# Kernel optimization log

Hardware: AMD Instinct MI355X
Metric: run time of the kernel (lower is better)

Reference implementation:

```python
import jax, jax.numpy as jnp
import numpy as np

DET_SIZE = 5120
DET_THRESHOLD = 0.5
NMS_THRESHOLD = 0.4
STRIDES = (8, 16, 32)
NUM_ANCHORS = 2
TOP_K = 2048  # fixed pre-NMS candidate count (jit-friendly stand-in for torch.where filtering)


def _anchor_centers(stride):
    n = DET_SIZE // stride
    g = jnp.arange(n, dtype=jnp.float32) * stride
    X, Y = jnp.meshgrid(g, g, indexing='xy')       # matches torch.meshgrid(..., indexing='xy')
    c = jnp.stack([X, Y], axis=-1).reshape(-1, 2)  # (n*n, 2), x fastest
    return jnp.repeat(c, NUM_ANCHORS, axis=0)      # stack([c]*2, dim=1).reshape(-1,2) == interleaved repeat


def _pairwise_iou(b):
    # b: (K,4) xyxy
    area = jnp.clip(b[:, 2] - b[:, 0], 0.0) * jnp.clip(b[:, 3] - b[:, 1], 0.0)
    lt = jnp.maximum(b[:, None, :2], b[None, :, :2])
    rb = jnp.minimum(b[:, None, 2:], b[None, :, 2:])
    wh = jnp.clip(rb - lt, 0.0)
    inter = wh[..., 0] * wh[..., 1]
    return inter / (area[:, None] + area[None, :] - inter + 1e-9)


def _forward(scores8, bbox8, lms8, scores16, bbox16, lms16, scores32, bbox32, lms32, det_scale):
    confs, boxes, lmss = [], [], []
    per_stride = [(scores8, bbox8, lms8), (scores16, bbox16, lms16), (scores32, bbox32, lms32)]
    for (conf, bbox, lms), stride in zip(per_stride, STRIDES):
        c = _anchor_centers(stride)                 # (N,2)
        b = bbox * stride                            # distance-style offsets scaled by stride
        l = lms * stride
        box = jnp.concatenate([c - b[:, :2], c + b[:, 2:4]], axis=-1) / det_scale  # (N,4) xyxy
        pts = (c[:, None, :] + l.reshape(-1, 5, 2)) / det_scale                    # (N,5,2)
        confs.append(conf.reshape(-1)); boxes.append(box); lmss.append(pts)
    conf = jnp.concatenate(confs)
    box = jnp.concatenate(boxes, axis=0)
    pts = jnp.concatenate(lmss, axis=0)
    # score threshold via masking (fixed shapes); below-threshold entries get conf=-1
    conf_m = jnp.where(conf >= DET_THRESHOLD, conf, -1.0)
    top_conf, top_idx = jax.lax.top_k(conf_m, TOP_K)
    top_box = box[top_idx]          # (K,4)
    top_pts = pts[top_idx]          # (K,5,2)
    valid = top_conf >= DET_THRESHOLD
    iou = _pairwise_iou(top_box)    # (K,K)
    later = jnp.arange(TOP_K)
    def body(i, keep):
        supp = (iou[i] > NMS_THRESHOLD) & (later > i) & keep[i] & valid[i]
        return keep & ~supp
    keep = jax.lax.fori_loop(0, TOP_K, body, valid)  # greedy NMS in descending-score order
    m = keep.astype(top_box.dtype)
    # (K, 15) = [conf | bbox(4) | lms(10)], suppressed/invalid rows zeroed
    return jnp.concatenate([(top_conf * m)[:, None], top_box * m[:, None], top_pts.reshape(TOP_K, 10) * m[:, None]], axis=-1)


def setup_inputs() -> dict:
    key = jax.random.key(0)
    ks = jax.random.split(key, 9)
    inp = {}
    for i, s in enumerate(STRIDES):
        n = DET_SIZE // s
        N = n * n * NUM_ANCHORS
        inp[f'scores{s}'] = jax.random.uniform(ks[3 * i], (N,), dtype=jnp.float32)
        inp[f'bbox{s}'] = jax.random.uniform(ks[3 * i + 1], (N, 4), dtype=jnp.float32) * 8.0
        inp[f'lms{s}'] = jax.random.normal(ks[3 * i + 2], (N, 10), dtype=jnp.float32) * 4.0
    inp['det_scale'] = jnp.array(0.5, dtype=jnp.float32)
    return inp


def reference(scores8, bbox8, lms8, scores16, bbox16, lms16, scores32, bbox32, lms32, det_scale):
    return _forward(scores8, bbox8, lms8, scores16, bbox16, lms16, scores32, bbox32, lms32, det_scale)
```

## Files before the change

### kernel.cpp

```cpp
#include <hip/hip_runtime.h>
#include <stdint.h>
#include <stddef.h>

#pragma clang fp contract(off)

#define N8   819200u
#define N16  204800u
#define N32  51200u
#define NTOT 1075200u
#define TOPK 2048
#define CAND_MAX 8192
#define NBIN 16384u
#define BINSHIFT 9
#define NMS_THR 0.4f
#define DET_THR 0.5f

#define OFF_HIST   0u
#define OFF_META   65536u
#define OFF_CAND   65600u
#define OFF_TIDX   131136u
#define OFF_TCONF  139328u
#define OFF_BOX    147520u
#define OFF_KEEP   180544u
#define OFF_DIAG   180800u
#define OFF_SUPP   188992u

__device__ __forceinline__ float load_conf(unsigned a, const float* __restrict__ s8,
                                           const float* __restrict__ s16,
                                           const float* __restrict__ s32) {
  if (a < N8) return s8[a];
  if (a < N8 + N16) return s16[a - N8];
  return s32[a - (N8 + N16)];
}

__device__ __forceinline__ void decode(unsigned a,
    const float* __restrict__ b8, const float* __restrict__ l8,
    const float* __restrict__ b16, const float* __restrict__ l16,
    const float* __restrict__ b32, const float* __restrict__ l32,
    float& cx, float& cy, float& s, const float*& bb, const float*& lm) {
  if (a < N8) {
    unsigned cell = a >> 1;
    cx = (float)((cell % 640u) * 8u); cy = (float)((cell / 640u) * 8u);
    s = 8.f; bb = b8 + (size_t)a * 4; lm = l8 + (size_t)a * 10;
  } else if (a < N8 + N16) {
    unsigned loc = a - N8; unsigned cell = loc >> 1;
    cx = (float)((cell % 320u) * 16u); cy = (float)((cell / 320u) * 16u);
    s = 16.f; bb = b16 + (size_t)loc * 4; lm = l16 + (size_t)loc * 10;
  } else {
    unsigned loc = a - (N8 + N16); unsigned cell = loc >> 1;
    cx = (float)((cell % 160u) * 32u); cy = (float)((cell / 160u) * 32u);
    s = 32.f; bb = b32 + (size_t)loc * 4; lm = l32 + (size_t)loc * 10;
  }
}

__global__ void k_hist(const float* __restrict__ s8, const float* __restrict__ s16,
                       const float* __restrict__ s32, unsigned* __restrict__ hist) {
  unsigned i = blockIdx.x * blockDim.x + threadIdx.x;
  unsigned st = gridDim.x * blockDim.x;
  for (unsigned a = i; a < NTOT; a += st) {
    float c = load_conf(a, s8, s16, s32);
    if (c >= DET_THR) {
      unsigned v = (__float_as_uint(c) - 0x3F000000u) >> BINSHIFT;
      if (v > NBIN - 1u) v = NBIN - 1u;
      atomicAdd(&hist[v], 1u);
    }
  }
}

__global__ void __launch_bounds__(1024) k_scan(const unsigned* __restrict__ hist,
                                               unsigned* __restrict__ meta) {
  __shared__ unsigned suf[1024];
  int t = threadIdx.x;
  const unsigned* hp = hist + (size_t)t * 16;
  unsigned s = 0;
  for (int b = 0; b < 16; b++) s += hp[b];
  suf[t] = s;
  __syncthreads();
  for (int d = 1; d < 1024; d <<= 1) {
    unsigned v = (t + d < 1024) ? suf[t + d] : 0u;
    __syncthreads();
    suf[t] += v;
    __syncthreads();
  }
  unsigned total = suf[0];
  unsigned mine = suf[t];
  unsigned nxt = (t < 1023) ? suf[t + 1] : 0u;
  if (total < (unsigned)TOPK) {
    if (t == 0) { meta[0] = 0u; meta[2] = total; }
    return;
  }
  if (mine >= (unsigned)TOPK && nxt < (unsigned)TOPK) {
    unsigned run = nxt, cut = (unsigned)t * 16u;
    for (int b = 15; b >= 0; b--) {
      run += hp[b];
      if (run >= (unsigned)TOPK) { cut = (unsigned)t * 16u + (unsigned)b; break; }
    }
    meta[0] = cut; meta[2] = total;
  }
}

__global__ void k_compact(const float* __restrict__ s8, const float* __restrict__ s16,
                          const float* __restrict__ s32, unsigned* __restrict__ meta,
                          unsigned long long* __restrict__ cand) {
  unsigned cut = meta[0];
  unsigned i = blockIdx.x * blockDim.x + threadIdx.x;
  unsigned st = gridDim.x * blockDim.x;
  for (unsigned a = i; a < NTOT; a += st) {
    float c = load_conf(a, s8, s16, s32);
    if (c >= DET_THR) {
      unsigned b = __float_as_uint(c);
      unsigned v = (b - 0x3F000000u) >> BINSHIFT;
      if (v >= cut) {
        unsigned pos = atomicAdd(&meta[3], 1u);
        if (pos < (unsigned)CAND_MAX)
          cand[pos] = ((unsigned long long)b << 32) |
                      (unsigned long long)(0xFFFFFFFFu - a);
      }
    }
  }
}

__global__ void __launch_bounds__(256) k_rank(
    const unsigned long long* __restrict__ cand, const unsigned* __restrict__ meta,
    const float* __restrict__ b8, const float* __restrict__ l8,
    const float* __restrict__ b16, const float* __restrict__ l16,
    const float* __restrict__ b32, const float* __restrict__ l32,
    const float* __restrict__ dsp,
    unsigned* __restrict__ tidx, float* __restrict__ tconf, float* __restrict__ box) {
  unsigned count = meta[3];
  if (count > (unsigned)CAND_MAX) count = (unsigned)CAND_MAX;
  unsigned wave = blockIdx.x * 4u + (threadIdx.x >> 6);
  unsigned lane = threadIdx.x & 63u;
  if (wave >= count) return;
  unsigned long long my = cand[wave];
  unsigned cnt = 0;
  for (unsigned i = lane; i < count; i += 64u)
    cnt += (cand[i] > my) ? 1u : 0u;
  for (int d = 32; d > 0; d >>= 1) cnt += __shfl_down(cnt, d);
  if (lane == 0 && cnt < (unsigned)TOPK) {
    unsigned r = cnt;
    unsigned a = 0xFFFFFFFFu - (unsigned)(my & 0xFFFFFFFFull);
    float conf = __uint_as_float((unsigned)(my >> 32));
    float cx, cy, s; const float* bb; const float* lm;
    decode(a, b8, l8, b16, l16, b32, l32, cx, cy, s, bb, lm);
    float ds = dsp[0];
    float b0 = bb[0] * s, b1 = bb[1] * s, b2 = bb[2] * s, b3 = bb[3] * s;
    box[r * 4 + 0] = (cx - b0) / ds;
    box[r * 4 + 1] = (cy - b1) / ds;
    box[r * 4 + 2] = (cx + b2) / ds;
    box[r * 4 + 3] = (cy + b3) / ds;
    tidx[r] = a; tconf[r] = conf;
  }
}

__global__ void __launch_bounds__(256) k_supp(const float* __restrict__ box,
                                              unsigned long long* __restrict__ supp,
                                              unsigned* __restrict__ diag32) {
  int i = blockIdx.x;
  const float4 bi = ((const float4*)box)[i];
  float ai = fmaxf(bi.z - bi.x, 0.f) * fmaxf(bi.w - bi.y, 0.f);
  int tid = threadIdx.x;
  int lane = tid & 63, wv = tid >> 6;
  for (int base = 0; base < TOPK; base += 256) {
    int j = base + tid;
    const float4 bj = ((const float4*)box)[j];
    float aj = fmaxf(bj.z - bj.x, 0.f) * fmaxf(bj.w - bj.y, 0.f);
    float ltx = fmaxf(bi.x, bj.x), lty = fmaxf(bi.y, bj.y);
    float rbx = fminf(bi.z, bj.z), rby = fminf(bi.w, bj.w);
    float w = fmaxf(rbx - ltx, 0.f), h = fmaxf(rby - lty, 0.f);
    float inter = w * h;
    float iou = inter / (ai + aj - inter + 1e-9f);
    bool pred = (iou > NMS_THR) && (j > i);
    unsigned long long word = __ballot(pred);
    int w64 = (base >> 6) + wv;
    if (lane == 0) {
      supp[(size_t)i * 32 + w64] = word;
      if (w64 == (i >> 6))
        diag32[i] = (unsigned)(word >> (((i >> 5) & 1) * 32));
    }
  }
}

__global__ void __launch_bounds__(64) k_nms(const unsigned* __restrict__ supp32,
                                            const unsigned* __restrict__ diag32,
                                            const unsigned* __restrict__ meta,
                                            unsigned* __restrict__ keepmask) {
  int lane = threadIdx.x;
  unsigned count = meta[3];
  if (count > (unsigned)TOPK) count = (unsigned)TOPK;
  unsigned lo = (unsigned)lane * 32u;
  unsigned kw = (count >= lo + 32u) ? 0xFFFFFFFFu
              : (count <= lo ? 0u : ((1u << (count - lo)) - 1u));
  const unsigned* sp = supp32 + lane;
  unsigned T0[32], T1[32], T2[32], T3[32];
  unsigned dga[32], dgb[32];

#define LOADT(BUF, C)                                                         \
  _Pragma("unroll") for (int k = 0; k < 32; k++)                              \
      BUF[k] = sp[((size_t)(unsigned)((C) * 32 + k)) * 64];
#define LOADD(DBUF, C)                                                        \
  _Pragma("unroll") for (int k = 0; k < 32; k++)                              \
      DBUF[k] = diag32[(unsigned)((C) * 32 + k)];

  LOADT(T0, 0) LOADT(T1, 1) LOADT(T2, 2) LOADT(T3, 3)
  LOADD(dga, 0)

#define STEP(BUF, DCUR, DNXT, C)                                              \
  {                                                                           \
    unsigned w = __builtin_amdgcn_readlane(kw, (C));                          \
    _Pragma("unroll") for (int k = 0; k < 32; k++) {                          \
      unsigned t = ((w >> k) & 1u) ? DCUR[k] : 0u;                            \
      w &= ~t;                                                                \
    }                                                                         \
    if ((C) + 1 < 64) { LOADD(DNXT, (C) + 1) }                                \
    unsigned acc = 0u;                                                        \
    _Pragma("unroll") for (int k = 0; k < 32; k++) {                          \
      unsigned mk = (unsigned)((int)(w << (31 - k)) >> 31);                   \
      acc |= BUF[k] & mk;                                                     \
    }                                                                         \
    kw &= ~acc;                                                               \
    if ((C) + 4 < 64) { LOADT(BUF, (C) + 4) }                                 \
  }

#pragma unroll 1
  for (int c = 0; c < 64; c += 8) {
    STEP(T0, dga, dgb, c + 0)
    STEP(T1, dgb, dga, c + 1)
    STEP(T2, dga, dgb, c + 2)
    STEP(T3, dgb, dga, c + 3)
    STEP(T0, dga, dgb, c + 4)
    STEP(T1, dgb, dga, c + 5)
    STEP(T2, dga, dgb, c + 6)
    STEP(T3, dgb, dga, c + 7)
  }
#undef LOADT
#undef LOADD
#undef STEP
  keepmask[lane] = kw;
}

__global__ void __launch_bounds__(256) k_out(
    const unsigned* __restrict__ keepmask,
    const unsigned* __restrict__ tidx, const float* __restrict__ tconf,
    const float* __restrict__ b8, const float* __restrict__ l8,
    const float* __restrict__ b16, const float* __restrict__ l16,
    const float* __restrict__ b32, const float* __restrict__ l32,
    const float* __restrict__ dsp, float* __restrict__ out) {
  int r = blockIdx.x * 256 + threadIdx.x;
  if (r >= TOPK) return;
  bool kept = (keepmask[r >> 5] >> (r & 31)) & 1u;
  float o[15];
  if (kept) {
    unsigned a = tidx[r];
    float cx, cy, s; const float* bb; const float* lm;
    decode(a, b8, l8, b16, l16, b32, l32, cx, cy, s, bb, lm);
    float ds = dsp[0];
    o[0] = tconf[r];
    float b0 = bb[0] * s, b1 = bb[1] * s, b2 = bb[2] * s, b3 = bb[3] * s;
    o[1] = (cx - b0) / ds;
    o[2] = (cy - b1) / ds;
    o[3] = (cx + b2) / ds;
    o[4] = (cy + b3) / ds;
    for (int p = 0; p < 5; p++) {
      float lx = lm[2 * p] * s, ly = lm[2 * p + 1] * s;
      o[5 + 2 * p] = (cx + lx) / ds;
      o[6 + 2 * p] = (cy + ly) / ds;
    }
  } else {
    for (int c = 0; c < 15; c++) o[c] = 0.f;
  }
  for (int c = 0; c < 15; c++) out[(size_t)r * 15 + c] = o[c];
}

extern "C" void kernel_launch(void* const* d_in, const int* in_sizes, int n_in,
                              void* d_out, int out_size, void* d_ws, size_t ws_size,
                              hipStream_t stream) {
  const float* s8  = (const float*)d_in[0];
  const float* b8  = (const float*)d_in[1];
  const float* l8  = (const float*)d_in[2];
  const float* s16 = (const float*)d_in[3];
  const float* b16 = (const float*)d_in[4];
  const float* l16 = (const float*)d_in[5];
  const float* s32 = (const float*)d_in[6];
  const float* b32 = (const float*)d_in[7];
  const float* l32 = (const float*)d_in[8];
  const float* dsp = (const float*)d_in[9];
  char* ws = (char*)d_ws;
  unsigned* hist = (unsigned*)(ws + OFF_HIST);
  unsigned* meta = (unsigned*)(ws + OFF_META);
  unsigned long long* cand = (unsigned long long*)(ws + OFF_CAND);
  unsigned* tidx = (unsigned*)(ws + OFF_TIDX);
  float* tconf = (float*)(ws + OFF_TCONF);
  float* box = (float*)(ws + OFF_BOX);
  unsigned* keepm = (unsigned*)(ws + OFF_KEEP);
  unsigned* diag = (unsigned*)(ws + OFF_DIAG);
  unsigned long long* supp = (unsigned long long*)(ws + OFF_SUPP);
  float* out = (float*)d_out;

  hipMemsetAsync(ws, 0, OFF_META + 64, stream);
  k_hist<<<2048, 256, 0, stream>>>(s8, s16, s32, hist);
  k_scan<<<1, 1024, 0, stream>>>(hist, meta);
  k_compact<<<2048, 256, 0, stream>>>(s8, s16, s32, meta, cand);
  k_rank<<<CAND_MAX / 4, 256, 0, stream>>>(cand, meta, b8, l8, b16, l16, b32, l32,
                                           dsp, tidx, tconf, box);
  k_supp<<<TOPK, 256, 0, stream>>>(box, supp, diag);
  k_nms<<<1, 64, 0, stream>>>((const unsigned*)supp, diag, meta, keepm);
  k_out<<<8, 256, 0, stream>>>(keepm, tidx, tconf, b8, l8, b16, l16, b32, l32,
                               dsp, out);
}
```

Measured before the change: 119.9 us.

## Transpose suppression matrix for vectorized NMS loads, fuse NMS with output, halve histogram

```diff
diff --git a/kernel.cpp b/kernel.cpp
--- a/kernel.cpp
+++ b/kernel.cpp
@@ -10,20 +10,19 @@
 #define NTOT 1075200u
 #define TOPK 2048
 #define CAND_MAX 8192
-#define NBIN 16384u
-#define BINSHIFT 9
+#define NBIN 8192u
+#define BINSHIFT 10
 #define NMS_THR 0.4f
 #define DET_THR 0.5f
 
 #define OFF_HIST   0u
-#define OFF_META   65536u
-#define OFF_CAND   65600u
-#define OFF_TIDX   131136u
-#define OFF_TCONF  139328u
-#define OFF_BOX    147520u
-#define OFF_KEEP   180544u
-#define OFF_DIAG   180800u
-#define OFF_SUPP   188992u
+#define OFF_META   32768u
+#define OFF_CAND   32832u
+#define OFF_TIDX   98368u
+#define OFF_TCONF  106560u
+#define OFF_BOX    114752u
+#define OFF_DIAG   147520u
+#define OFF_SUPPT  155968u
 
 __device__ __forceinline__ float load_conf(unsigned a, const float* __restrict__ s8,
                                            const float* __restrict__ s16,
@@ -71,9 +70,9 @@
                                                unsigned* __restrict__ meta) {
   __shared__ unsigned suf[1024];
   int t = threadIdx.x;
-  const unsigned* hp = hist + (size_t)t * 16;
+  const unsigned* hp = hist + (size_t)t * 8;
   unsigned s = 0;
-  for (int b = 0; b < 16; b++) s += hp[b];
+  for (int b = 0; b < 8; b++) s += hp[b];
   suf[t] = s;
   __syncthreads();
   for (int d = 1; d < 1024; d <<= 1) {
@@ -90,10 +89,10 @@
     return;
   }
   if (mine >= (unsigned)TOPK && nxt < (unsigned)TOPK) {
-    unsigned run = nxt, cut = (unsigned)t * 16u;
-    for (int b = 15; b >= 0; b--) {
+    unsigned run = nxt, cut = (unsigned)t * 8u;
+    for (int b = 7; b >= 0; b--) {
       run += hp[b];
-      if (run >= (unsigned)TOPK) { cut = (unsigned)t * 16u + (unsigned)b; break; }
+      if (run >= (unsigned)TOPK) { cut = (unsigned)t * 8u + (unsigned)b; break; }
     }
     meta[0] = cut; meta[2] = total;
   }
@@ -154,13 +153,14 @@
 }
 
 __global__ void __launch_bounds__(256) k_supp(const float* __restrict__ box,
-                                              unsigned long long* __restrict__ supp,
+                                              unsigned* __restrict__ supp_t,
                                               unsigned* __restrict__ diag32) {
   int i = blockIdx.x;
   const float4 bi = ((const float4*)box)[i];
   float ai = fmaxf(bi.z - bi.x, 0.f) * fmaxf(bi.w - bi.y, 0.f);
   int tid = threadIdx.x;
   int lane = tid & 63, wv = tid >> 6;
+  int c = i >> 5, k = i & 31;
   for (int base = 0; base < TOPK; base += 256) {
     int j = base + tid;
     const float4 bj = ((const float4*)box)[j];
@@ -174,102 +174,109 @@
     unsigned long long word = __ballot(pred);
     int w64 = (base >> 6) + wv;
     if (lane == 0) {
-      supp[(size_t)i * 32 + w64] = word;
+      supp_t[c * 2048 + (2 * w64) * 32 + k]     = (unsigned)(word & 0xFFFFFFFFull);
+      supp_t[c * 2048 + (2 * w64 + 1) * 32 + k] = (unsigned)(word >> 32);
       if (w64 == (i >> 6))
         diag32[i] = (unsigned)(word >> (((i >> 5) & 1) * 32));
     }
   }
 }
 
-__global__ void __launch_bounds__(64) k_nms(const unsigned* __restrict__ supp32,
-                                            const unsigned* __restrict__ diag32,
-                                            const unsigned* __restrict__ meta,
-                                            unsigned* __restrict__ keepmask) {
-  int lane = threadIdx.x;
-  unsigned count = meta[3];
-  if (count > (unsigned)TOPK) count = (unsigned)TOPK;
-  unsigned lo = (unsigned)lane * 32u;
-  unsigned kw = (count >= lo + 32u) ? 0xFFFFFFFFu
-              : (count <= lo ? 0u : ((1u << (count - lo)) - 1u));
-  const unsigned* sp = supp32 + lane;
-  unsigned T0[32], T1[32], T2[32], T3[32];
-  unsigned dga[32], dgb[32];
-
-#define LOADT(BUF, C)                                                         \
-  _Pragma("unroll") for (int k = 0; k < 32; k++)                              \
-      BUF[k] = sp[((size_t)(unsigned)((C) * 32 + k)) * 64];
-#define LOADD(DBUF, C)                                                        \
-  _Pragma("unroll") for (int k = 0; k < 32; k++)                              \
-      DBUF[k] = diag32[(unsigned)((C) * 32 + k)];
-
-  LOADT(T0, 0) LOADT(T1, 1) LOADT(T2, 2) LOADT(T3, 3)
-  LOADD(dga, 0)
-
-#define STEP(BUF, DCUR, DNXT, C)                                              \
-  {                                                                           \
-    unsigned w = __builtin_amdgcn_readlane(kw, (C));                          \
-    _Pragma("unroll") for (int k = 0; k < 32; k++) {                          \
-      unsigned t = ((w >> k) & 1u) ? DCUR[k] : 0u;                            \
-      w &= ~t;                                                                \
-    }                                                                         \
-    if ((C) + 1 < 64) { LOADD(DNXT, (C) + 1) }                                \
-    unsigned acc = 0u;                                                        \
-    _Pragma("unroll") for (int k = 0; k < 32; k++) {                          \
-      unsigned mk = (unsigned)((int)(w << (31 - k)) >> 31);                   \
-      acc |= BUF[k] & mk;                                                     \
-    }                                                                         \
-    kw &= ~acc;                                                               \
-    if ((C) + 4 < 64) { LOADT(BUF, (C) + 4) }                                 \
-  }
-
-#pragma unroll 1
-  for (int c = 0; c < 64; c += 8) {
-    STEP(T0, dga, dgb, c + 0)
-    STEP(T1, dgb, dga, c + 1)
-    STEP(T2, dga, dgb, c + 2)
-    STEP(T3, dgb, dga, c + 3)
-    STEP(T0, dga, dgb, c + 4)
-    STEP(T1, dgb, dga, c + 5)
-    STEP(T2, dga, dgb, c + 6)
-    STEP(T3, dgb, dga, c + 7)
-  }
-#undef LOADT
-#undef LOADD
-#undef STEP
-  keepmask[lane] = kw;
-}
-
-__global__ void __launch_bounds__(256) k_out(
-    const unsigned* __restrict__ keepmask,
+__global__ void __launch_bounds__(256) k_nms_out(
+    const unsigned* __restrict__ supp_t, const unsigned* __restrict__ diag32,
+    const unsigned* __restrict__ meta,
     const unsigned* __restrict__ tidx, const float* __restrict__ tconf,
     const float* __restrict__ b8, const float* __restrict__ l8,
     const float* __restrict__ b16, const float* __restrict__ l16,
     const float* __restrict__ b32, const float* __restrict__ l32,
     const float* __restrict__ dsp, float* __restrict__ out) {
-  int r = blockIdx.x * 256 + threadIdx.x;
-  if (r >= TOPK) return;
-  bool kept = (keepmask[r >> 5] >> (r & 31)) & 1u;
-  float o[15];
-  if (kept) {
-    unsigned a = tidx[r];
-    float cx, cy, s; const float* bb; const float* lm;
-    decode(a, b8, l8, b16, l16, b32, l32, cx, cy, s, bb, lm);
-    float ds = dsp[0];
-    o[0] = tconf[r];
-    float b0 = bb[0] * s, b1 = bb[1] * s, b2 = bb[2] * s, b3 = bb[3] * s;
-    o[1] = (cx - b0) / ds;
-    o[2] = (cy - b1) / ds;
-    o[3] = (cx + b2) / ds;
-    o[4] = (cy + b3) / ds;
-    for (int p = 0; p < 5; p++) {
-      float lx = lm[2 * p] * s, ly = lm[2 * p + 1] * s;
-      o[5 + 2 * p] = (cx + lx) / ds;
-      o[6 + 2 * p] = (cy + ly) / ds;
-    }
-  } else {
-    for (int c = 0; c < 15; c++) o[c] = 0.f;
-  }
-  for (int c = 0; c < 15; c++) out[(size_t)r * 15 + c] = o[c];
+  __shared__ unsigned keepw[64];
+  int tid = threadIdx.x;
+  if (tid < 64) {
+    int lane = tid;
+    unsigned count = meta[3];
+    if (count > (unsigned)TOPK) count = (unsigned)TOPK;
+    unsigned lo = (unsigned)lane * 32u;
+    unsigned kw = (count >= lo + 32u) ? 0xFFFFFFFFu
+                : (count <= lo ? 0u : ((1u << (count - lo)) - 1u));
+    const uint4* rp4 = (const uint4*)supp_t + (size_t)lane * 8;
+    uint4 T0[8], T1[8], T2[8], T3[8];
+    unsigned dga[32], dgb[32];
+
+#define LOADT(BUF, C)                                                         \
+  _Pragma("unroll") for (int q = 0; q < 8; q++)                               \
+      BUF[q] = rp4[(size_t)((C) * 512 + q)];
+#define LOADD(DBUF, C)                                                        \
+  _Pragma("unroll") for (int k = 0; k < 32; k++)                              \
+      DBUF[k] = diag32[(unsigned)((C) * 32 + k)];
+
+    LOADT(T0, 0) LOADT(T1, 1) LOADT(T2, 2) LOADT(T3, 3)
+    LOADD(dga, 0)
+
+#define STEP(BUF, DCUR, DNXT, C)                                              \
+  {                                                                           \
+    unsigned w = __builtin_amdgcn_readlane(kw, (C));                          \
+    _Pragma("unroll") for (int k = 0; k < 32; k++) {                          \
+      unsigned d = __builtin_amdgcn_readfirstlane(DCUR[k]);                   \
+      w &= ~(((w >> k) & 1u) ? d : 0u);                                       \
+    }                                                                         \
+    if ((C) + 1 < 64) { LOADD(DNXT, (C) + 1) }                                \
+    unsigned acc = 0u;                                                        \
+    _Pragma("unroll") for (int q = 0; q < 8; q++) {                           \
+      unsigned m0 = (unsigned)((int)(w << (31 - (4 * q + 0))) >> 31);         \
+      unsigned m1 = (unsigned)((int)(w << (31 - (4 * q + 1))) >> 31);         \
+      unsigned m2 = (unsigned)((int)(w << (31 - (4 * q + 2))) >> 31);         \
+      unsigned m3 = (unsigned)((int)(w << (31 - (4 * q + 3))) >> 31);         \
+      acc |= BUF[q].x & m0;                                                   \
+      acc |= BUF[q].y & m1;                                                   \
+      acc |= BUF[q].z & m2;                                                   \
+      acc |= BUF[q].w & m3;                                                   \
+    }                                                                         \
+    kw &= ~acc;                                                               \
+    if ((C) + 4 < 64) { LOADT(BUF, (C) + 4) }                                 \
+  }
+
+#pragma unroll 1
+    for (int c = 0; c < 64; c += 8) {
+      STEP(T0, dga, dgb, c + 0)
+      STEP(T1, dgb, dga, c + 1)
+      STEP(T2, dga, dgb, c + 2)
+      STEP(T3, dgb, dga, c + 3)
+      STEP(T0, dga, dgb, c + 4)
+      STEP(T1, dgb, dga, c + 5)
+      STEP(T2, dga, dgb, c + 6)
+      STEP(T3, dgb, dga, c + 7)
+    }
+#undef LOADT
+#undef LOADD
+#undef STEP
+    keepw[lane] = kw;
+  }
+  __syncthreads();
+  float ds = dsp[0];
+  for (int r = tid; r < TOPK; r += 256) {
+    bool kept = (keepw[r >> 5] >> (r & 31)) & 1u;
+    float o[15];
+    if (kept) {
+      unsigned a = tidx[r];
+      float cx, cy, s; const float* bb; const float* lm;
+      decode(a, b8, l8, b16, l16, b32, l32, cx, cy, s, bb, lm);
+      o[0] = tconf[r];
+      float b0 = bb[0] * s, b1 = bb[1] * s, b2 = bb[2] * s, b3 = bb[3] * s;
+      o[1] = (cx - b0) / ds;
+      o[2] = (cy - b1) / ds;
+      o[3] = (cx + b2) / ds;
+      o[4] = (cy + b3) / ds;
+      for (int p = 0; p < 5; p++) {
+        float lx = lm[2 * p] * s, ly = lm[2 * p + 1] * s;
+        o[5 + 2 * p] = (cx + lx) / ds;
+        o[6 + 2 * p] = (cy + ly) / ds;
+      }
+    } else {
+      for (int cc = 0; cc < 15; cc++) o[cc] = 0.f;
+    }
+    for (int cc = 0; cc < 15; cc++) out[(size_t)r * 15 + cc] = o[cc];
+  }
 }
 
 extern "C" void kernel_launch(void* const* d_in, const int* in_sizes, int n_in,
@@ -292,9 +299,8 @@
   unsigned* tidx = (unsigned*)(ws + OFF_TIDX);
   float* tconf = (float*)(ws + OFF_TCONF);
   float* box = (float*)(ws + OFF_BOX);
-  unsigned* keepm = (unsigned*)(ws + OFF_KEEP);
   unsigned* diag = (unsigned*)(ws + OFF_DIAG);
-  unsigned long long* supp = (unsigned long long*)(ws + OFF_SUPP);
+  unsigned* supp_t = (unsigned*)(ws + OFF_SUPPT);
   float* out = (float*)d_out;
 
   hipMemsetAsync(ws, 0, OFF_META + 64, stream);
@@ -303,8 +309,7 @@
   k_compact<<<2048, 256, 0, stream>>>(s8, s16, s32, meta, cand);
   k_rank<<<CAND_MAX / 4, 256, 0, stream>>>(cand, meta, b8, l8, b16, l16, b32, l32,
                                            dsp, tidx, tconf, box);
-  k_supp<<<TOPK, 256, 0, stream>>>(box, supp, diag);
-  k_nms<<<1, 64, 0, stream>>>((const unsigned*)supp, diag, meta, keepm);
-  k_out<<<8, 256, 0, stream>>>(keepm, tidx, tconf, b8, l8, b16, l16, b32, l32,
-                               dsp, out);
-}
+  k_supp<<<TOPK, 256, 0, stream>>>(box, supp_t, diag);
+  k_nms_out<<<1, 256, 0, stream>>>(supp_t, diag, meta, tidx, tconf,
+                                   b8, l8, b16, l16, b32, l32, dsp, out);
+}
```

Measured after the change: 123.5 us. +3.0%, slower.
